# Kernel optimization log

Hardware: AMD Instinct MI355X
Metric: run time of the kernel (lower is better)

Reference implementation:

```python
import jax, jax.numpy as jnp
import numpy as np

B, S, D, H, BLEN, FF = 4, 4096, 1024, 16, 256, 4096
DH = D // H
NEG = -1e9
EPS = 1e-6


def setup_inputs() -> dict:
    key = jax.random.key(0)
    ks = jax.random.split(key, 8)
    s = 0.02
    return {
        "X": jax.random.normal(ks[0], (B, S, D), jnp.float32),
        "Wq": jax.random.normal(ks[1], (D, D), jnp.float32) * s,
        "Wk": jax.random.normal(ks[2], (D, D), jnp.float32) * s,
        "Wv": jax.random.normal(ks[3], (D, D), jnp.float32) * s,
        "Wo": jax.random.normal(ks[4], (D, D), jnp.float32) * s,
        "g_attn": jnp.ones((D,), jnp.float32),
        "b_attn": jnp.zeros((D,), jnp.float32),
        "W1": jax.random.normal(ks[5], (D, FF), jnp.float32) * s,
        "b1": jnp.zeros((FF,), jnp.float32),
        "W2": jax.random.normal(ks[6], (FF, D), jnp.float32) * s,
        "b2": jnp.zeros((D,), jnp.float32),
        "g_ffn": jnp.ones((D,), jnp.float32),
        "b_ffn": jnp.zeros((D,), jnp.float32),
    }


def _layernorm(x, g, b):
    mu = jnp.mean(x, axis=-1, keepdims=True)
    var = jnp.mean(jnp.square(x - mu), axis=-1, keepdims=True)
    return (x - mu) * jax.lax.rsqrt(var + EPS) * g + b


def _local_attn(X, Wq, Wk, Wv, Wo):
    def split_heads(y):  # [B,S,D] -> [B,H,S,DH]
        return y.reshape(B, S, H, DH).transpose(0, 2, 1, 3)

    q = split_heads(X @ Wq) * (DH ** -0.5)
    k = split_heads(X @ Wk)
    v = split_heads(X @ Wv)

    nb = S // BLEN  # S is a multiple of BLEN, so the torch pad is a no-op
    q = q.reshape(B, H, nb, BLEN, DH)
    k = k.reshape(B, H, nb, BLEN, DH)
    v = v.reshape(B, H, nb, BLEN, DH)

    # First block: plain causal attention within block 0.
    causal = NEG * jnp.triu(jnp.ones((BLEN, BLEN), jnp.float32), 1)
    logits0 = jnp.einsum('bhkd,bhqd->bhqk', k[:, :, 0], q[:, :, 0]) + causal
    out0 = jax.nn.softmax(logits0, axis=-1) @ v[:, :, 0]  # [B,H,BLEN,DH]

    # Tail blocks attend to [previous block, current block].
    local_k = jnp.concatenate([k[:, :, :-1], k[:, :, 1:]], axis=3)  # [B,H,nb-1,2B,DH]
    local_v = jnp.concatenate([v[:, :, :-1], v[:, :, 1:]], axis=3)
    tail_q = q[:, :, 1:]
    bias = NEG * jnp.triu(jnp.ones((BLEN, 2 * BLEN), jnp.float32), BLEN + 1)
    logits = jnp.einsum('bhnkd,bhnqd->bhnqk', local_k, tail_q) + bias
    tail = jnp.einsum('bhnqk,bhnkd->bhnqd', jax.nn.softmax(logits, axis=-1), local_v)
    tail = tail.reshape(B, H, S - BLEN, DH)

    res = jnp.concatenate([out0, tail], axis=2)       # [B,H,S,DH]
    res = res.transpose(0, 2, 1, 3).reshape(B, S, D)  # merge heads
    return res @ Wo


def reference(X, Wq, Wk, Wv, Wo, g_attn, b_attn, W1, b1, W2, b2, g_ffn, b_ffn):
    y = _local_attn(X, Wq, Wk, Wv, Wo)
    X = _layernorm(y + X, g_attn, b_attn)
    y = jax.nn.relu(X @ W1 + b1) @ W2 + b2
    X = _layernorm(y + X, g_ffn, b_ffn)
    return X
```

## Files before the change

kernel.cpp:

```cpp
#include <hip/hip_runtime.h>
#include <stdint.h>

#define B_    4
#define S_    4096
#define D_    1024
#define H_    16
#define DH_   64
#define BLEN_ 256
#define FF_   4096
#define M_    16384

typedef unsigned short u16;
typedef __attribute__((ext_vector_type(8))) short s8v;
typedef __attribute__((ext_vector_type(4))) short s4v;
typedef __attribute__((ext_vector_type(4))) float f4v;

#define MFMA32(A,B,C) __builtin_amdgcn_mfma_f32_16x16x32_bf16(A,B,C,0,0,0)
#define BAR() asm volatile("s_barrier" ::: "memory")

__device__ __forceinline__ f4v mfma16(s4v a, s4v b, f4v c) {
#if defined(__HIP_DEVICE_COMPILE__)
#if __has_builtin(__builtin_amdgcn_mfma_f32_16x16x16bf16_1k)
  return __builtin_amdgcn_mfma_f32_16x16x16bf16_1k(a, b, c, 0, 0, 0);
#elif __has_builtin(__builtin_amdgcn_mfma_f32_16x16x16_bf16_1k)
  return __builtin_amdgcn_mfma_f32_16x16x16_bf16_1k(a, b, c, 0, 0, 0);
#elif __has_builtin(__builtin_amdgcn_mfma_f32_16x16x16_bf16)
  return __builtin_amdgcn_mfma_f32_16x16x16_bf16(a, b, c, 0, 0, 0);
#else
  f4v d;
  asm volatile("v_mfma_f32_16x16x16_bf16 %0, %1, %2, %3"
               : "=v"(d) : "v"(a), "v"(b), "v"(c));
  return d;
#endif
#else
  (void)a; (void)b; return c;
#endif
}

__device__ __forceinline__ u16 f2b(float f) {
  union { float f; unsigned u; } v; v.f = f;
  unsigned r = v.u + 0x7fffu + ((v.u >> 16) & 1u);
  return (u16)(r >> 16);
}
__device__ __forceinline__ float b2f(u16 h) {
  union { unsigned u; float f; } v; v.u = ((unsigned)h) << 16; return v.f;
}

__device__ __forceinline__ void gld16(const void* gp, void* lp) {
  __builtin_amdgcn_global_load_lds(
      (const __attribute__((address_space(1))) void*)(uintptr_t)gp,
      (__attribute__((address_space(3))) void*)(uintptr_t)lp, 16, 0, 0);
}


__global__ __launch_bounds__(256) void k_castx(const float* __restrict__ in, u16* __restrict__ out) {
  long i = (long)blockIdx.x * 256 + threadIdx.x;
  float4 v = ((const float4*)in)[i];
  s4v o; o[0] = (short)f2b(v.x); o[1] = (short)f2b(v.y);
  o[2] = (short)f2b(v.z); o[3] = (short)f2b(v.w);
  *(s4v*)(out + i * 4) = o;
}

__global__ __launch_bounds__(256) void k_wt(const float* __restrict__ in, u16* __restrict__ out,
                                            int K, int N, float scale) {
  __shared__ u16 tile[32][33];
  const int tx = threadIdx.x & 31, ty = threadIdx.x >> 5;
  const int kb = blockIdx.y << 5, nb = blockIdx.x << 5;
#pragma unroll
  for (int r = 0; r < 4; r++) {
    int row = ty + r * 8;
    tile[row][tx] = f2b(in[(long)(kb + row) * N + nb + tx] * scale);
  }
  __syncthreads();
#pragma unroll
  for (int r = 0; r < 4; r++) {
    int row = ty + r * 8;
    out[(long)(nb + row) * K + kb + tx] = tile[tx][row];
  }
}

template<int QM, int QN>
__device__ __forceinline__ void phmfma(f4v (&acc)[8][4], s8v (&A)[4][2], s8v (&B)[2][2]) {
#pragma unroll
  for (int mt = 0; mt < 4; mt++)
#pragma unroll
    for (int nt = 0; nt < 2; nt++) {
      acc[QM * 4 + mt][QN * 2 + nt] = MFMA32(A[mt][0], B[nt][0], acc[QM * 4 + mt][QN * 2 + nt]);
      acc[QM * 4 + mt][QN * 2 + nt] = MFMA32(A[mt][1], B[nt][1], acc[QM * 4 + mt][QN * 2 + nt]);
    }
}

#define RD_A(d, half, DST) \
  _Pragma("unroll") for (int mt = 0; mt < 4; mt++) { \
    DST[mt][0] = rdA(d, mt + (half) * 4, 0); DST[mt][1] = rdA(d, mt + (half) * 4, 1); }
#define RD_B(d, half, DST) \
  _Pragma("unroll") for (int nt = 0; nt < 2; nt++) { \
    DST[nt][0] = rdB(d, nt + (half) * 2, 0); DST[nt][1] = rdB(d, nt + (half) * 2, 1); }

#define PHASE(GATE, READS, STAGE, QM, QN, AA, BB) \
  READS STAGE \
  BAR(); \
  asm volatile("s_waitcnt lgkmcnt(0)" ::: "memory"); \
  __builtin_amdgcn_sched_barrier(0); \
  __builtin_amdgcn_s_setprio(1); \
  phmfma<QM, QN>(acc, AA, BB); \
  __builtin_amdgcn_s_setprio(0); \
  asm volatile("s_waitcnt vmcnt(" #GATE ")" ::: "memory"); \
  BAR();

template<int EPI, int K>
__global__ __launch_bounds__(512, 2) void k_gemm256(
    const u16* __restrict__ A, const u16* __restrict__ Bt,
    const float* __restrict__ bias, const void* __restrict__ res,
    u16* __restrict__ out, int N) {
  __shared__ __align__(16) u16 sA[2][16384];
  __shared__ __align__(16) u16 sB[2][16384];
  const int t = threadIdx.x, lane = t & 63, w = t >> 6;
  const int wm = w >> 2, wn = w & 3;
  const int nwg = gridDim.x, cpx = nwg >> 3, orig = blockIdx.x;
  const int wg = (orig & 7) * cpx + (orig >> 3);
  const int mb = wg & 63, nb = wg >> 6;
  const int m0 = mb << 8, n0 = nb << 8;
  constexpr int NT = K >> 6;
  constexpr int NP = NT >> 1;

  const int srow = lane >> 3;
  const int scol = ((lane & 7) ^ srow) << 3;
  const u16* gA = A + (size_t)(m0 + srow) * K + scol;
  const u16* gB = Bt + (size_t)(n0 + srow) * K + scol;

  auto stA = [&](int d, int h, int kt) {
#pragma unroll
    for (int i = 0; i < 2; i++) {
      int c = i * 8 + w;
      gld16(gA + (size_t)(h * 128 + c * 8) * K + kt * 64, &sA[d][h * 8192 + c * 512]);
    }
  };
  auto stB = [&](int d, int h, int kt) {
#pragma unroll
    for (int i = 0; i < 2; i++) {
      int c = i * 8 + w;
      gld16(gB + (size_t)(h * 128 + c * 8) * K + kt * 64, &sB[d][h * 8192 + c * 512]);
    }
  };

  const int swz = (lane & 7) << 4;
  const int g8b = (lane >> 4) << 4;
  const int r16 = lane & 15;
  auto rdA = [&](int d, int mt, int kh) -> s8v {
    int byt = (mt * 32 + wm * 16 + r16) * 128 + ((kh * 64 + g8b) ^ swz);
    return *(const s8v*)((const char*)sA[d] + byt);
  };
  auto rdB = [&](int d, int nt, int kh) -> s8v {
    int byt = (nt * 64 + wn * 16 + r16) * 128 + ((kh * 64 + g8b) ^ swz);
    return *(const s8v*)((const char*)sB[d] + byt);
  };

  f4v acc[8][4];
  f4v zz = {0.f, 0.f, 0.f, 0.f};
#pragma unroll
  for (int i = 0; i < 8; i++)
#pragma unroll
    for (int j = 0; j < 4; j++) acc[i][j] = zz;

  stA(0, 0, 0); stB(0, 0, 0); stB(0, 1, 0); stA(0, 1, 0);
  stA(1, 0, 1); stB(1, 0, 1); stB(1, 1, 1);
  asm volatile("s_waitcnt vmcnt(10)" ::: "memory");
  BAR();

  s8v a0[4][2], a1[4][2], bb0[2][2], bb1[2][2];

  for (int pp = 0; pp < NP - 1; ++pp) {
    const int j = pp * 2;
    PHASE(10, RD_A(0, 0, a0) RD_B(0, 0, bb0), stA(1, 1, j + 1);, 0, 0, a0, bb0)
    PHASE(10, RD_B(0, 1, bb1),                stA(0, 0, j + 2);, 0, 1, a0, bb1)
    PHASE(10, RD_A(0, 1, a1),                 stB(0, 0, j + 2);, 1, 0, a1, bb0)
    PHASE(10, ,                               stB(0, 1, j + 2);, 1, 1, a1, bb1)
    PHASE(10, RD_A(1, 0, a0) RD_B(1, 0, bb0), stA(0, 1, j + 2);, 0, 0, a0, bb0)
    PHASE(10, RD_B(1, 1, bb1),                stA(1, 0, j + 3);, 0, 1, a0, bb1)
    PHASE(10, RD_A(1, 1, a1),                 stB(1, 0, j + 3);, 1, 0, a1, bb0)
    PHASE(10, ,                               stB(1, 1, j + 3);, 1, 1, a1, bb1)
  }
  PHASE(10, RD_A(0, 0, a0) RD_B(0, 0, bb0), stA(1, 1, NT - 1);, 0, 0, a0, bb0)
  PHASE(8,  RD_B(0, 1, bb1),                ,                   0, 1, a0, bb1)
  PHASE(8,  RD_A(0, 1, a1),                 ,                   1, 0, a1, bb0)
  PHASE(4,  ,                               ,                   1, 1, a1, bb1)
  PHASE(2,  RD_A(1, 0, a0) RD_B(1, 0, bb0), ,                   0, 0, a0, bb0)
  PHASE(0,  RD_B(1, 1, bb1),                ,                   0, 1, a0, bb1)
  PHASE(0,  RD_A(1, 1, a1),                 ,                   1, 0, a1, bb0)
  PHASE(0,  ,                               ,                   1, 1, a1, bb1)

  const int g4 = (lane >> 4) << 2;
#pragma unroll
  for (int mt = 0; mt < 8; mt++) {
#pragma unroll
    for (int nt = 0; nt < 4; nt++) {
      const int col = n0 + nt * 64 + wn * 16 + r16;
      const long rbase = m0 + mt * 32 + wm * 16 + g4;
      float bcol = 0.f;
      if constexpr (EPI == 2 || EPI == 3) bcol = bias[col];
#pragma unroll
      for (int r = 0; r < 4; r++) {
        long idx = (rbase + r) * (long)N + col;
        float v = acc[mt][nt][r];
        if constexpr (EPI == 1) v += ((const float*)res)[idx];
        if constexpr (EPI == 2) { v += bcol; v = fmaxf(v, 0.f); }
        if constexpr (EPI == 3) { v += bcol + b2f(((const u16*)res)[idx]); }
        out[idx] = f2b(v);
      }
    }
  }
}

__global__ __launch_bounds__(256) void k_attn(const u16* __restrict__ QKV, u16* __restrict__ Aout) {
  __shared__ __align__(16) u16 sK[64 * 64];
  __shared__ __align__(16) u16 sVT[64 * 64];
  const int t = threadIdx.x, lane = t & 63, w = t >> 6;
  const int qblock = blockIdx.x;
  const int b = blockIdx.y >> 4, h = blockIdx.y & 15;
  const int qcol = lane & 15, g = lane >> 4, g4 = g << 2;
  const int win = (qblock == 0) ? 0 : (qblock - 1) * BLEN_;
  const int nch = (qblock == 0) ? 4 : 8;
  const int qbw = qblock * BLEN_ + w * 64;
  const long rowbase = (long)b * S_;
  const int LDQ = 3072;

  s8v qf[4][2];
#pragma unroll
  for (int nt = 0; nt < 4; nt++)
#pragma unroll
    for (int kh = 0; kh < 2; kh++)
      qf[nt][kh] = *(const s8v*)(QKV + (rowbase + qbw + nt * 16 + qcol) * LDQ + h * DH_ + kh * 32 + (g << 3));

  f4v zz = {0.f, 0.f, 0.f, 0.f};
  f4v acc[4][4];
#pragma unroll
  for (int i = 0; i < 4; i++)
#pragma unroll
    for (int j = 0; j < 4; j++) acc[i][j] = zz;
  float mrow[4] = {-1e30f, -1e30f, -1e30f, -1e30f};
  float lrow[4] = {0.f, 0.f, 0.f, 0.f};

  for (int c = 0; c < nch; ++c) {
    const int kb = win + c * 64;
    __syncthreads();
#pragma unroll
    for (int p = 0; p < 2; p++) {
      int key = p * 32 + (t >> 3);
      int d8 = (t & 7) << 3;
      s8v kv = *(const s8v*)(QKV + (rowbase + kb + key) * LDQ + 1024 + h * DH_ + d8);
      int bo = key * 128 + d8 * 2; bo ^= (key & 7) << 4;
      *(s8v*)((char*)sK + bo) = kv;
    }
#pragma unroll
    for (int p = 0; p < 2; p++) {
      int key = (t & 31) + (p << 5);
      int d8 = (t >> 5) << 3;
      s8v vv = *(const s8v*)(QKV + (rowbase + kb + key) * LDQ + 2048 + h * DH_ + d8);
#pragma unroll
      for (int j = 0; j < 8; j++) {
        int dh = d8 + j;
        int bo = dh * 128 + key * 2; bo ^= (dh & 7) << 3;
        *(u16*)((char*)sVT + bo) = (u16)vv[j];
      }
    }
    __syncthreads();
    if (kb > qbw + 63) continue;

    f4v st[4][4];
#pragma unroll
    for (int i = 0; i < 4; i++)
#pragma unroll
      for (int j = 0; j < 4; j++) st[i][j] = zz;
#pragma unroll
    for (int kh = 0; kh < 2; kh++) {
#pragma unroll
      for (int mt = 0; mt < 4; mt++) {
        int key = mt * 16 + qcol;
        int bo = key * 128 + kh * 64 + (g << 4); bo ^= (key & 7) << 4;
        s8v kf = *(const s8v*)((const char*)sK + bo);
#pragma unroll
        for (int nt = 0; nt < 4; nt++) st[mt][nt] = MFMA32(kf, qf[nt][kh], st[mt][nt]);
      }
    }
    if (kb + 63 > qbw) {
#pragma unroll
      for (int mt = 0; mt < 4; mt++) {
        int kbase = kb + mt * 16 + g4;
#pragma unroll
        for (int nt = 0; nt < 4; nt++) {
          int qabs = qbw + nt * 16 + qcol;
#pragma unroll
          for (int r = 0; r < 4; r++)
            if (kbase + r > qabs) st[mt][nt][r] = -1e30f;
        }
      }
    }
    s4v pf[4][4];
#pragma unroll
    for (int nt = 0; nt < 4; nt++) {
      float cm = -1e30f;
#pragma unroll
      for (int mt = 0; mt < 4; mt++)
#pragma unroll
        for (int r = 0; r < 4; r++) cm = fmaxf(cm, st[mt][nt][r]);
      cm = fmaxf(cm, __shfl_xor(cm, 16));
      cm = fmaxf(cm, __shfl_xor(cm, 32));
      float mnew = fmaxf(mrow[nt], cm);
      float sc = __expf(mrow[nt] - mnew);
      mrow[nt] = mnew;
      float ps = 0.f;
#pragma unroll
      for (int kt = 0; kt < 4; kt++) {
        s4v pp;
#pragma unroll
        for (int r = 0; r < 4; r++) {
          float sv = st[kt][nt][r];
          float p = (sv > -1e29f) ? __expf(sv - mnew) : 0.f;
          ps += p;
          pp[r] = (short)f2b(p);
        }
        pf[nt][kt] = pp;
      }
      ps += __shfl_xor(ps, 16);
      ps += __shfl_xor(ps, 32);
      lrow[nt] = lrow[nt] * sc + ps;
#pragma unroll
      for (int dt = 0; dt < 4; dt++) acc[dt][nt] *= sc;
    }
#pragma unroll
    for (int dt = 0; dt < 4; dt++) {
      int dh = dt * 16 + qcol;
#pragma unroll
      for (int kt = 0; kt < 4; kt++) {
        int bo = dh * 128 + kt * 32 + (g << 3); bo ^= (dh & 7) << 3;
        s4v vf = *(const s4v*)((const char*)sVT + bo);
#pragma unroll
        for (int nt = 0; nt < 4; nt++) acc[dt][nt] = mfma16(vf, pf[nt][kt], acc[dt][nt]);
      }
    }
  }

#pragma unroll
  for (int nt = 0; nt < 4; nt++) {
    float inv = 1.f / lrow[nt];
    long qrow = rowbase + qbw + nt * 16 + qcol;
#pragma unroll
    for (int dt = 0; dt < 4; dt++) {
      s4v o;
#pragma unroll
      for (int r = 0; r < 4; r++) o[r] = (short)f2b(acc[dt][nt][r] * inv);
      *(s4v*)(Aout + qrow * D_ + h * DH_ + dt * 16 + g4) = o;
    }
  }
}

template<int OUTB>
__global__ __launch_bounds__(256) void k_ln(const u16* __restrict__ in, const float* __restrict__ gw,
                                            const float* __restrict__ bw, float* __restrict__ outf,
                                            u16* __restrict__ outb) {
  const int t = threadIdx.x, lane = t & 63, w = t >> 6;
  const long base = (long)blockIdx.x * D_;
  s4v xv = *(const s4v*)(in + base + t * 4);
  float v0 = b2f((u16)xv[0]), v1 = b2f((u16)xv[1]), v2 = b2f((u16)xv[2]), v3 = b2f((u16)xv[3]);
  float s = v0 + v1 + v2 + v3;
  float s2 = v0 * v0 + v1 * v1 + v2 * v2 + v3 * v3;
#pragma unroll
  for (int off = 1; off < 64; off <<= 1) { s += __shfl_xor(s, off); s2 += __shfl_xor(s2, off); }
  __shared__ float red[8];
  if (lane == 0) { red[w] = s; red[4 + w] = s2; }
  __syncthreads();
  s = red[0] + red[1] + red[2] + red[3];
  s2 = red[4] + red[5] + red[6] + red[7];
  float mu = s * (1.f / D_);
  float var = s2 * (1.f / D_) - mu * mu;
  float rstd = rsqrtf(var + 1e-6f);
  float4 gv = ((const float4*)gw)[t];
  float4 bv = ((const float4*)bw)[t];
  float o0 = (v0 - mu) * rstd * gv.x + bv.x;
  float o1 = (v1 - mu) * rstd * gv.y + bv.y;
  float o2 = (v2 - mu) * rstd * gv.z + bv.z;
  float o3 = (v3 - mu) * rstd * gv.w + bv.w;
  if constexpr (OUTB) {
    s4v o; o[0] = (short)f2b(o0); o[1] = (short)f2b(o1); o[2] = (short)f2b(o2); o[3] = (short)f2b(o3);
    *(s4v*)(outb + base + t * 4) = o;
  } else {
    float4 o; o.x = o0; o.y = o1; o.z = o2; o.w = o3;
    *(float4*)(outf + base + t * 4) = o;
  }
}


extern "C" void kernel_launch(void* const* d_in, const int* in_sizes, int n_in,
                              void* d_out, int out_size, void* d_ws, size_t ws_size,
                              hipStream_t stream) {
  const float* X      = (const float*)d_in[0];
  const float* Wq     = (const float*)d_in[1];
  const float* Wk     = (const float*)d_in[2];
  const float* Wv     = (const float*)d_in[3];
  const float* Wo     = (const float*)d_in[4];
  const float* g_attn = (const float*)d_in[5];
  const float* b_attn = (const float*)d_in[6];
  const float* W1     = (const float*)d_in[7];
  const float* b1     = (const float*)d_in[8];
  const float* W2     = (const float*)d_in[9];
  const float* b2     = (const float*)d_in[10];
  const float* g_ffn  = (const float*)d_in[11];
  const float* b_ffn  = (const float*)d_in[12];
  float* out = (float*)d_out;

  char* ws = (char*)d_ws;
  const size_t MB = 1ull << 20;
  u16* WqkvT = (u16*)(ws + 0 * MB);
  u16* WoT   = (u16*)(ws + 6 * MB);
  u16* W1T   = (u16*)(ws + 8 * MB);
  u16* W2T   = (u16*)(ws + 16 * MB);
  u16* Xb    = (u16*)(ws + 24 * MB);
  u16* QKVb  = (u16*)(ws + 56 * MB);
  u16* Ab    = (u16*)(ws + 152 * MB);
  u16* Yb    = (u16*)(ws + 184 * MB);
  u16* Mid   = QKVb;

  dim3 b256(256), b512(512);
  k_wt<<<dim3(32, 32),  b256, 0, stream>>>(Wq, WqkvT,               1024, 1024, 0.125f);
  k_wt<<<dim3(32, 32),  b256, 0, stream>>>(Wk, WqkvT + 1024 * 1024, 1024, 1024, 1.0f);
  k_wt<<<dim3(32, 32),  b256, 0, stream>>>(Wv, WqkvT + 2048 * 1024, 1024, 1024, 1.0f);
  k_wt<<<dim3(32, 32),  b256, 0, stream>>>(Wo, WoT, 1024, 1024, 1.0f);
  k_wt<<<dim3(128, 32), b256, 0, stream>>>(W1, W1T, 1024, 4096, 1.0f);
  k_wt<<<dim3(32, 128), b256, 0, stream>>>(W2, W2T, 4096, 1024, 1.0f);
  k_castx<<<dim3(16384), b256, 0, stream>>>(X, Xb);

  k_gemm256<0, 1024><<<dim3(768), b512, 0, stream>>>(Xb, WqkvT, nullptr, nullptr, QKVb, 3072);
  k_attn<<<dim3(16, B_ * H_), b256, 0, stream>>>(QKVb, Ab);
  k_gemm256<1, 1024><<<dim3(256), b512, 0, stream>>>(Ab, WoT, nullptr, X, Yb, 1024);
  k_ln<1><<<dim3(16384), b256, 0, stream>>>(Yb, g_attn, b_attn, nullptr, Xb);
  k_gemm256<2, 1024><<<dim3(1024), b512, 0, stream>>>(Xb, W1T, b1, nullptr, Mid, 4096);
  k_gemm256<3, 4096><<<dim3(256), b512, 0, stream>>>(Mid, W2T, b2, Xb, Yb, 1024);
  k_ln<0><<<dim3(16384), b256, 0, stream>>>(Yb, g_ffn, b_ffn, out, nullptr);

  (void)in_sizes; (void)n_in; (void)out_size; (void)ws_size;
}
```

Measured before the change: 602.4 us.

## Replace 8-phase GEMM schedule with triple-buffered K=32 tile pipeline

The 256x256 bf16 GEMM main loop used a hand-scheduled 8-phase ping-pong with K=64 double buffers and per-phase barriers. It now uses K=32 tiles in a three-slot rotating LDS ring with a new XOR swizzle. Each iteration prefetches two steps ahead, computes the whole 8x4 MFMA tile, then does one barrier. This halves barriers per K-step and simplifies scheduling, but each sync covers less MFMA work and loses the fine-grained overlap of LDS reads with MFMAs.

```diff
diff --git a/kernel.cpp b/kernel.cpp
--- a/kernel.cpp
+++ b/kernel.cpp
@@ -79,81 +79,51 @@
   }
 }
 
-template<int QM, int QN>
-__device__ __forceinline__ void phmfma(f4v (&acc)[8][4], s8v (&A)[4][2], s8v (&B)[2][2]) {
-#pragma unroll
-  for (int mt = 0; mt < 4; mt++)
-#pragma unroll
-    for (int nt = 0; nt < 2; nt++) {
-      acc[QM * 4 + mt][QN * 2 + nt] = MFMA32(A[mt][0], B[nt][0], acc[QM * 4 + mt][QN * 2 + nt]);
-      acc[QM * 4 + mt][QN * 2 + nt] = MFMA32(A[mt][1], B[nt][1], acc[QM * 4 + mt][QN * 2 + nt]);
-    }
-}
-
-#define RD_A(d, half, DST) \
-  _Pragma("unroll") for (int mt = 0; mt < 4; mt++) { \
-    DST[mt][0] = rdA(d, mt + (half) * 4, 0); DST[mt][1] = rdA(d, mt + (half) * 4, 1); }
-#define RD_B(d, half, DST) \
-  _Pragma("unroll") for (int nt = 0; nt < 2; nt++) { \
-    DST[nt][0] = rdB(d, nt + (half) * 2, 0); DST[nt][1] = rdB(d, nt + (half) * 2, 1); }
-
-#define PHASE(GATE, READS, STAGE, QM, QN, AA, BB) \
-  READS STAGE \
-  BAR(); \
-  asm volatile("s_waitcnt lgkmcnt(0)" ::: "memory"); \
-  __builtin_amdgcn_sched_barrier(0); \
-  __builtin_amdgcn_s_setprio(1); \
-  phmfma<QM, QN>(acc, AA, BB); \
-  __builtin_amdgcn_s_setprio(0); \
-  asm volatile("s_waitcnt vmcnt(" #GATE ")" ::: "memory"); \
-  BAR();
-
 template<int EPI, int K>
 __global__ __launch_bounds__(512, 2) void k_gemm256(
     const u16* __restrict__ A, const u16* __restrict__ Bt,
     const float* __restrict__ bias, const void* __restrict__ res,
     u16* __restrict__ out, int N) {
-  __shared__ __align__(16) u16 sA[2][16384];
-  __shared__ __align__(16) u16 sB[2][16384];
+  __shared__ __align__(16) u16 sAm[3][8192];
+  __shared__ __align__(16) u16 sBm[3][8192];
   const int t = threadIdx.x, lane = t & 63, w = t >> 6;
   const int wm = w >> 2, wn = w & 3;
   const int nwg = gridDim.x, cpx = nwg >> 3, orig = blockIdx.x;
   const int wg = (orig & 7) * cpx + (orig >> 3);
   const int mb = wg & 63, nb = wg >> 6;
   const int m0 = mb << 8, n0 = nb << 8;
-  constexpr int NT = K >> 6;
-  constexpr int NP = NT >> 1;
-
-  const int srow = lane >> 3;
-  const int scol = ((lane & 7) ^ srow) << 3;
-  const u16* gA = A + (size_t)(m0 + srow) * K + scol;
-  const u16* gB = Bt + (size_t)(n0 + srow) * K + scol;
-
-  auto stA = [&](int d, int h, int kt) {
+  constexpr int NT = K >> 5;
+
+  const int srow = lane >> 2;
+  const int ssl  = (lane & 3) ^ ((srow & 3) ^ ((srow >> 2) & 3));
+  const u16* gA = A + (size_t)(m0 + srow) * K + ssl * 8;
+  const u16* gB = Bt + (size_t)(n0 + srow) * K + ssl * 8;
+
+  auto stA = [&](u16* dst, int kt) {
 #pragma unroll
     for (int i = 0; i < 2; i++) {
       int c = i * 8 + w;
-      gld16(gA + (size_t)(h * 128 + c * 8) * K + kt * 64, &sA[d][h * 8192 + c * 512]);
+      gld16(gA + (size_t)(c * 16) * K + kt * 32, dst + c * 512);
     }
   };
-  auto stB = [&](int d, int h, int kt) {
+  auto stB = [&](u16* dst, int kt) {
 #pragma unroll
     for (int i = 0; i < 2; i++) {
       int c = i * 8 + w;
-      gld16(gB + (size_t)(h * 128 + c * 8) * K + kt * 64, &sB[d][h * 8192 + c * 512]);
+      gld16(gB + (size_t)(c * 16) * K + kt * 32, dst + c * 512);
     }
   };
 
-  const int swz = (lane & 7) << 4;
-  const int g8b = (lane >> 4) << 4;
-  const int r16 = lane & 15;
-  auto rdA = [&](int d, int mt, int kh) -> s8v {
-    int byt = (mt * 32 + wm * 16 + r16) * 128 + ((kh * 64 + g8b) ^ swz);
-    return *(const s8v*)((const char*)sA[d] + byt);
+  const int g = lane >> 4, r16 = lane & 15;
+  const int rsw = (r16 & 3) ^ ((r16 >> 2) & 3);
+  const int slotb = (g ^ rsw) << 4;
+  auto rdA = [&](const u16* base, int mt) -> s8v {
+    int byt = (mt * 32 + wm * 16 + r16) * 64 + slotb;
+    return *(const s8v*)((const char*)base + byt);
   };
-  auto rdB = [&](int d, int nt, int kh) -> s8v {
-    int byt = (nt * 64 + wn * 16 + r16) * 128 + ((kh * 64 + g8b) ^ swz);
-    return *(const s8v*)((const char*)sB[d] + byt);
+  auto rdB = [&](const u16* base, int nt) -> s8v {
+    int byt = (nt * 64 + wn * 16 + r16) * 64 + slotb;
+    return *(const s8v*)((const char*)base + byt);
   };
 
   f4v acc[8][4];
@@ -163,32 +133,43 @@
 #pragma unroll
     for (int j = 0; j < 4; j++) acc[i][j] = zz;
 
-  stA(0, 0, 0); stB(0, 0, 0); stB(0, 1, 0); stA(0, 1, 0);
-  stA(1, 0, 1); stB(1, 0, 1); stB(1, 1, 1);
-  asm volatile("s_waitcnt vmcnt(10)" ::: "memory");
+  auto compute = [&](const u16* a, const u16* b) {
+    s8v av[8], bv[4];
+#pragma unroll
+    for (int mt = 0; mt < 8; mt++) av[mt] = rdA(a, mt);
+#pragma unroll
+    for (int nt = 0; nt < 4; nt++) bv[nt] = rdB(b, nt);
+    __builtin_amdgcn_s_setprio(1);
+#pragma unroll
+    for (int mt = 0; mt < 8; mt++)
+#pragma unroll
+      for (int nt = 0; nt < 4; nt++)
+        acc[mt][nt] = MFMA32(av[mt], bv[nt], acc[mt][nt]);
+    __builtin_amdgcn_s_setprio(0);
+  };
+
+  u16 *aR = (u16*)sAm[0], *aN = (u16*)sAm[1], *aS = (u16*)sAm[2];
+  u16 *bR = (u16*)sBm[0], *bN = (u16*)sBm[1], *bS = (u16*)sBm[2];
+
+  stA(aR, 0); stB(bR, 0);
+  stA(aN, 1); stB(bN, 1);
+  asm volatile("s_waitcnt vmcnt(4)" ::: "memory");
   BAR();
 
-  s8v a0[4][2], a1[4][2], bb0[2][2], bb1[2][2];
-
-  for (int pp = 0; pp < NP - 1; ++pp) {
-    const int j = pp * 2;
-    PHASE(10, RD_A(0, 0, a0) RD_B(0, 0, bb0), stA(1, 1, j + 1);, 0, 0, a0, bb0)
-    PHASE(10, RD_B(0, 1, bb1),                stA(0, 0, j + 2);, 0, 1, a0, bb1)
-    PHASE(10, RD_A(0, 1, a1),                 stB(0, 0, j + 2);, 1, 0, a1, bb0)
-    PHASE(10, ,                               stB(0, 1, j + 2);, 1, 1, a1, bb1)
-    PHASE(10, RD_A(1, 0, a0) RD_B(1, 0, bb0), stA(0, 1, j + 2);, 0, 0, a0, bb0)
-    PHASE(10, RD_B(1, 1, bb1),                stA(1, 0, j + 3);, 0, 1, a0, bb1)
-    PHASE(10, RD_A(1, 1, a1),                 stB(1, 0, j + 3);, 1, 0, a1, bb0)
-    PHASE(10, ,                               stB(1, 1, j + 3);, 1, 1, a1, bb1)
-  }
-  PHASE(10, RD_A(0, 0, a0) RD_B(0, 0, bb0), stA(1, 1, NT - 1);, 0, 0, a0, bb0)
-  PHASE(8,  RD_B(0, 1, bb1),                ,                   0, 1, a0, bb1)
-  PHASE(8,  RD_A(0, 1, a1),                 ,                   1, 0, a1, bb0)
-  PHASE(4,  ,                               ,                   1, 1, a1, bb1)
-  PHASE(2,  RD_A(1, 0, a0) RD_B(1, 0, bb0), ,                   0, 0, a0, bb0)
-  PHASE(0,  RD_B(1, 1, bb1),                ,                   0, 1, a0, bb1)
-  PHASE(0,  RD_A(1, 1, a1),                 ,                   1, 0, a1, bb0)
-  PHASE(0,  ,                               ,                   1, 1, a1, bb1)
+  for (int j = 0; j < NT - 2; ++j) {
+    stA(aS, j + 2); stB(bS, j + 2);
+    compute(aR, bR);
+    asm volatile("s_waitcnt vmcnt(4)" ::: "memory");
+    BAR();
+    u16* ta = aS; aS = aR; aR = aN; aN = ta;
+    u16* tb = bS; bS = bR; bR = bN; bN = tb;
+  }
+  compute(aR, bR);
+  asm volatile("s_waitcnt vmcnt(0)" ::: "memory");
+  BAR();
+  { u16* ta = aS; aS = aR; aR = aN; aN = ta;
+    u16* tb = bS; bS = bR; bR = bN; bN = tb; }
+  compute(aR, bR);
 
   const int g4 = (lane >> 4) << 2;
 #pragma unroll
```

After: 671.0 us. +11.4%, slower.
